# Optimization experiments

Hardware: AMD Instinct MI355X
Metric: run time of the kernel (lower is better)

The kernel has to match this reference:

```python
import math
import jax, jax.numpy as jnp
import numpy as np

B, T, C, H = 4, 1024, 1024, 16


def setup_inputs() -> dict:
    key = jax.random.key(0)
    k1, k2, k3 = jax.random.split(key, 3)
    scale = 0.02
    return {
        "x": jax.random.normal(k1, (B, T, C), dtype=jnp.float32),
        "w_attn": jax.random.normal(k2, (C, 3 * C), dtype=jnp.float32) * scale,
        "b_attn": jnp.zeros((3 * C,), dtype=jnp.float32),
        "w_proj": jax.random.normal(k3, (C, C), dtype=jnp.float32) * scale,
        "b_proj": jnp.zeros((C,), dtype=jnp.float32),
    }


def reference(x, w_attn, b_attn, w_proj, b_proj):
    b, t, c = x.shape
    h = H
    d = c // h
    qkv = x @ w_attn + b_attn                      # [b, t, 3c]
    q, k, v = jnp.split(qkv, 3, axis=-1)
    # [b, h, t, d]
    q = q.reshape(b, t, h, d).transpose(0, 2, 1, 3)
    k = k.reshape(b, t, h, d).transpose(0, 2, 1, 3)
    v = v.reshape(b, t, h, d).transpose(0, 2, 1, 3)
    att = jnp.einsum("bhqd,bhkd->bhqk", q, k) * (1.0 / math.sqrt(d))
    causal = jnp.tril(jnp.ones((t, t), dtype=bool))
    att = jnp.where(causal[None, None], att, -jnp.inf)
    att = jax.nn.softmax(att, axis=-1)
    # dropout is identity in eval mode
    y = jnp.einsum("bhqk,bhkd->bhqd", att, v)      # [b, h, t, d]
    y = y.transpose(0, 2, 1, 3).reshape(b, t, c)
    return y @ w_proj + b_proj
```

## Files before the change

### kernel.cpp

```cpp
#include <hip/hip_runtime.h>

typedef __bf16 bf16;
typedef float f32x4 __attribute__((ext_vector_type(4)));
typedef bf16 bf16x4 __attribute__((ext_vector_type(4)));
typedef bf16 bf16x8 __attribute__((ext_vector_type(8)));

#define MFMA16(a, b, c) __builtin_amdgcn_mfma_f32_16x16x32_bf16((a), (b), (c), 0, 0, 0)

__device__ __forceinline__ f32x4 zero4() {
    f32x4 z; z[0] = 0.f; z[1] = 0.f; z[2] = 0.f; z[3] = 0.f; return z;
}
__device__ __forceinline__ void gl_lds16(const bf16* g, bf16* l) {
    __builtin_amdgcn_global_load_lds(
        (const __attribute__((address_space(1))) void*)g,
        (__attribute__((address_space(3))) void*)l, 16, 0, 0);
}

__global__ __launch_bounds__(256) void conv_k(const float* __restrict__ src,
                                              bf16* __restrict__ dst, int n)
{
    const int i = (blockIdx.x * 256 + threadIdx.x) * 8;
    if (i >= n) return;
    const float4 a = *(const float4*)(src + i);
    const float4 b = *(const float4*)(src + i + 4);
    bf16x8 o;
    o[0] = (bf16)a.x; o[1] = (bf16)a.y; o[2] = (bf16)a.z; o[3] = (bf16)a.w;
    o[4] = (bf16)b.x; o[5] = (bf16)b.y; o[6] = (bf16)b.z; o[7] = (bf16)b.w;
    *(bf16x8*)(dst + i) = o;
}

__global__ __launch_bounds__(256) void transp_k(const float* __restrict__ src,
                                                bf16* __restrict__ dst, int K, int N)
{
    __shared__ bf16 Ls[64][72];
    const int tid = threadIdx.x;
    const int k0 = blockIdx.y << 6;
    const int n0 = blockIdx.x << 6;
    #pragma unroll
    for (int it = 0; it < 4; ++it) {
        const int lin = (it << 10) + (tid << 2);
        const int r = lin >> 6, c = lin & 63;
        const float4 v = *(const float4*)(src + (size_t)(k0 + r) * N + n0 + c);
        bf16x4 o; o[0] = (bf16)v.x; o[1] = (bf16)v.y; o[2] = (bf16)v.z; o[3] = (bf16)v.w;
        *(bf16x4*)&Ls[r][c] = o;
    }
    __syncthreads();
    #pragma unroll
    for (int it = 0; it < 2; ++it) {
        const int lin = (it << 11) + (tid << 3);
        const int nn = lin >> 6, kk = lin & 63;
        bf16x8 o;
        #pragma unroll
        for (int j = 0; j < 8; ++j) o[j] = Ls[kk + j][nn];
        *(bf16x8*)(dst + (size_t)(n0 + nn) * K + k0 + kk) = o;
    }
}

template <int MODE, int BN>
__global__ __launch_bounds__(256)
void gemm_bt(const bf16* __restrict__ A, const bf16* __restrict__ Bt,
             const float* __restrict__ bias,
             bf16* __restrict__ qw, bf16* __restrict__ kw, bf16* __restrict__ vw,
             float* __restrict__ outf, int M, int N, int K)
{
    constexpr int BK = 32;
    constexpr int MF = (BN == 128) ? 4 : 2;
    constexpr int NF = 4;
    constexpr int AE = 128 * BK;
    constexpr int BE = BN * BK;
    constexpr int LPI = (BN == 128) ? 4 : 3;

    __shared__ __align__(16) bf16 smem[3 * (AE + BE)];
    bf16* const Asb = smem;
    bf16* const Bsb = smem + 3 * AE;

    const int tid  = threadIdx.x;
    const int lane = tid & 63;
    const int wid  = tid >> 6;
    const int l16  = lane & 15;
    const int g    = lane >> 4;
    const int wrb  = (BN == 128) ? ((wid >> 1) << 6) : (wid << 5);
    const int wcb  = (BN == 128) ? ((wid & 1) << 6) : 0;

    const int p   = blockIdx.x;
    const int xcd = p & 7;
    const int r   = p >> 3;
    int by, bx;
    if (MODE == 0) { by = ((xcd >> 1) << 3) + r / 12; bx = (xcd & 1) * 12 + r % 12; }
    else           { by = ((xcd >> 1) << 3) + (r >> 3); bx = ((xcd & 1) << 3) + (r & 7); }
    const int m0 = by << 7;
    const int n0 = bx * BN;

    const int srow = lane >> 2;
    const int schk = lane & 3;
    const int rA0 = (wid << 5) + srow;
    const int rA1 = rA0 + 16;
    const int rB0 = wid * (BN / 4) + srow;
    const int rB1 = rB0 + 16;
    const bf16* pa0 = A  + (size_t)(m0 + rA0) * K + ((schk ^ ((rA0 >> 1) & 3)) << 3);
    const bf16* pa1 = A  + (size_t)(m0 + rA1) * K + ((schk ^ ((rA1 >> 1) & 3)) << 3);
    const bf16* pb0 = Bt + (size_t)(n0 + rB0) * K + ((schk ^ ((rB0 >> 1) & 3)) << 3);
    const bf16* pb1 = Bt + (size_t)(n0 + rB1) * K + ((schk ^ ((rB1 >> 1) & 3)) << 3);
    const int dA0 = (wid << 5) * BK, dA1 = dA0 + 16 * BK;
    const int dB0 = (wid * (BN / 4)) * BK, dB1 = dB0 + 16 * BK;

    auto issue = [&](bf16* ab, bf16* bb) {
        gl_lds16(pa0, ab + dA0); gl_lds16(pa1, ab + dA1);
        gl_lds16(pb0, bb + dB0);
        if constexpr (BN == 128) gl_lds16(pb1, bb + dB1);
        pa0 += BK; pa1 += BK; pb0 += BK; pb1 += BK;
    };

    int offA[MF], offB[NF];
    #pragma unroll
    for (int mf = 0; mf < MF; ++mf) {
        const int rr = wrb + (mf << 4) + l16;
        offA[mf] = rr * BK + ((g ^ ((rr >> 1) & 3)) << 3);
    }
    #pragma unroll
    for (int nf = 0; nf < NF; ++nf) {
        const int rr = wcb + (nf << 4) + l16;
        offB[nf] = rr * BK + ((g ^ ((rr >> 1) & 3)) << 3);
    }

    f32x4 acc[MF][NF];
    #pragma unroll
    for (int i = 0; i < MF; ++i)
        #pragma unroll
        for (int j = 0; j < NF; ++j) acc[i][j] = zero4();

    const int nk = K >> 5;
    issue(Asb, Bsb);
    issue(Asb + AE, Bsb + BE);

    for (int kt = 0; kt < nk; ++kt) {
        if (kt == nk - 1) {
            asm volatile("s_waitcnt vmcnt(0)" ::: "memory");
        } else {
            if constexpr (LPI == 4) asm volatile("s_waitcnt vmcnt(4)" ::: "memory");
            else                    asm volatile("s_waitcnt vmcnt(3)" ::: "memory");
        }
        __builtin_amdgcn_s_barrier();
        const int nxt = kt + 2;
        if (nxt < nk) {
            const int s = nxt - (nxt / 3) * 3;
            issue(Asb + s * AE, Bsb + s * BE);
        }
        const int c = kt - (kt / 3) * 3;
        const bf16* ac = Asb + c * AE;
        const bf16* bc = Bsb + c * BE;
        bf16x8 af[MF], bfr[NF];
        #pragma unroll
        for (int mf = 0; mf < MF; ++mf) af[mf] = *(const bf16x8*)&ac[offA[mf]];
        #pragma unroll
        for (int nf = 0; nf < NF; ++nf) bfr[nf] = *(const bf16x8*)&bc[offB[nf]];
        __builtin_amdgcn_s_setprio(1);
        #pragma unroll
        for (int mf = 0; mf < MF; ++mf)
            #pragma unroll
            for (int nf = 0; nf < NF; ++nf)
                acc[mf][nf] = MFMA16(af[mf], bfr[nf], acc[mf][nf]);
        __builtin_amdgcn_s_setprio(0);
    }
    __syncthreads();

    if (MODE == 0) {
        bf16* const Es = smem;
        const int bq  = m0 >> 10;
        const int tb  = m0 & 1023;
        const int hh0 = (n0 & 1023) >> 6;
        const bool isV = (n0 >= 2048);
        if (isV) {
            #pragma unroll
            for (int mf = 0; mf < MF; ++mf)
                #pragma unroll
                for (int nf = 0; nf < NF; ++nf) {
                    const int nn = wcb + (nf << 4) + l16;
                    const float bs = bias[n0 + nn];
                    bf16x4 pq;
                    #pragma unroll
                    for (int j = 0; j < 4; ++j) pq[j] = (bf16)(acc[mf][nf][j] + bs);
                    const int m = wrb + (mf << 4) + (g << 2);
                    const int pp = ((m >> 5) << 5) + (((m >> 2) & 3) << 3) + (((m >> 4) & 1) << 2);
                    *(bf16x4*)&Es[nn * 128 + pp] = pq;
                }
        } else {
            #pragma unroll
            for (int mf = 0; mf < MF; ++mf)
                #pragma unroll
                for (int nf = 0; nf < NF; ++nf) {
                    const int nn = wcb + (nf << 4) + l16;
                    const float bs = bias[n0 + nn];
                    #pragma unroll
                    for (int j = 0; j < 4; ++j) {
                        const int mm = wrb + (mf << 4) + (g << 2) + j;
                        Es[mm * 128 + nn] = (bf16)(acc[mf][nf][j] + bs);
                    }
                }
        }
        __syncthreads();
        #pragma unroll
        for (int it = 0; it < 8; ++it) {
            const int idx = (it << 8) + tid;
            const int row = idx >> 4, ch = idx & 15;
            const bf16x8 v = *(const bf16x8*)&Es[row * 128 + (ch << 3)];
            if (isV) {
                const int dd = row & 63, hh = hh0 + (row >> 6);
                *(bf16x8*)(vw + ((size_t)((bq << 4) + hh) << 16) + ((size_t)dd << 10)
                           + tb + (ch << 3)) = v;
            } else {
                const int t = tb + row;
                const int cc = ch << 3;
                const int hh = hh0 + (cc >> 6);
                bf16* const dst = (n0 < 1024) ? qw : kw;
                *(bf16x8*)(dst + ((size_t)((bq << 4) + hh) << 16) + ((size_t)t << 6)
                           + (cc & 63)) = v;
            }
        }
    } else {
        #pragma unroll
        for (int mf = 0; mf < MF; ++mf)
            #pragma unroll
            for (int nf = 0; nf < NF; ++nf) {
                const int ng = n0 + wcb + (nf << 4) + l16;
                const float bs = bias[ng];
                #pragma unroll
                for (int j = 0; j < 4; ++j) {
                    const int mg = m0 + wrb + (mf << 4) + (g << 2) + j;
                    outf[(size_t)mg * N + ng] = acc[mf][nf][j] + bs;
                }
            }
    }
}

__global__ __launch_bounds__(256)
void attn_k(const bf16* __restrict__ Qp, const bf16* __restrict__ Kp,
            const bf16* __restrict__ Vt, bf16* __restrict__ att)
{
    __shared__ __align__(16) bf16 Kl0[64 * 64], Kl1[64 * 64];
    __shared__ __align__(16) bf16 Vl0[64 * 64], Vl1[64 * 64];

    const int bh = blockIdx.x;
    const int bx = blockIdx.y;
    const int b  = bh >> 4, h = bh & 15;

    const int tid  = threadIdx.x;
    const int lane = tid & 63;
    const int wid  = tid >> 6;
    const int g    = lane >> 4;
    const int l16  = lane & 15;
    const int g8   = g << 3;

    const size_t hb = (size_t)bh << 16;
    const bf16* Qh = Qp + hb;
    const bf16* Kh = Kp + hb;
    const bf16* Vh = Vt + hb;

    const int srow = lane >> 3;
    const int sswz = ((lane & 7) ^ srow) << 3;
    const int kr0  = (wid << 4) + srow;
    const int kr1  = kr0 + 8;
    const int dst0 = (wid << 4) << 6;
    const int dst1 = ((wid << 4) + 8) << 6;

    int offKV[2][4];
    #pragma unroll
    for (int ks = 0; ks < 2; ++ks)
        #pragma unroll
        for (int cb = 0; cb < 4; ++cb) {
            const int r = (cb << 4) + l16;
            offKV[ks][cb] = (r << 6) + (((((ks << 2) + g)) ^ (r & 7)) << 3);
        }

    const float QSCALE = 0.125f * 1.44269504f;

    const int q1b = bx;
    const int q2b = 15 - bx;
    const int nkt = q2b;
    const int qloc = (wid << 4) + l16;

    const bf16* qp1 = Qh + ((size_t)((q1b << 6) + qloc) << 6) + g8;
    const bf16* qp2 = Qh + ((size_t)((q2b << 6) + qloc) << 6) + g8;
    bf16x8 q1f0 = *(const bf16x8*)qp1, q1f1 = *(const bf16x8*)(qp1 + 32);
    bf16x8 q2f0 = *(const bf16x8*)qp2, q2f1 = *(const bf16x8*)(qp2 + 32);
    #pragma unroll
    for (int e = 0; e < 8; ++e) {
        q1f0[e] = (bf16)(QSCALE * (float)q1f0[e]);
        q1f1[e] = (bf16)(QSCALE * (float)q1f1[e]);
        q2f0[e] = (bf16)(QSCALE * (float)q2f0[e]);
        q2f1[e] = (bf16)(QSCALE * (float)q2f1[e]);
    }

    f32x4 acc1[4], acc2[4];
    float m1 = -1e30f, l1 = 0.f, m2 = -1e30f, l2 = 0.f;
    #pragma unroll
    for (int i = 0; i < 4; ++i) { acc1[i] = zero4(); acc2[i] = zero4(); }

    gl_lds16(Kh + ((size_t)kr0 << 6) + sswz, Kl0 + dst0);
    gl_lds16(Kh + ((size_t)kr1 << 6) + sswz, Kl0 + dst1);
    gl_lds16(Vh + ((size_t)kr0 << 10) + sswz, Vl0 + dst0);
    gl_lds16(Vh + ((size_t)kr1 << 10) + sswz, Vl0 + dst1);
    __syncthreads();

    for (int kt = 0; kt <= nkt; ++kt) {
        const bool odd = kt & 1;
        if (kt < nkt) {
            const int kv1 = (kt + 1) << 6;
            bf16* Kn = odd ? Kl0 : Kl1;
            bf16* Vn = odd ? Vl0 : Vl1;
            gl_lds16(Kh + ((size_t)(kv1 + kr0) << 6) + sswz, Kn + dst0);
            gl_lds16(Kh + ((size_t)(kv1 + kr1) << 6) + sswz, Kn + dst1);
            gl_lds16(Vh + ((size_t)kr0 << 10) + kv1 + sswz, Vn + dst0);
            gl_lds16(Vh + ((size_t)kr1 << 10) + kv1 + sswz, Vn + dst1);
        }
        const bf16* Kc = odd ? Kl1 : Kl0;
        const bf16* Vc = odd ? Vl1 : Vl0;

        bf16x8 kf[2][4];
        #pragma unroll
        for (int ks = 0; ks < 2; ++ks)
            #pragma unroll
            for (int cb = 0; cb < 4; ++cb)
                kf[ks][cb] = *(const bf16x8*)&Kc[offKV[ks][cb]];

        {
            f32x4 sacc[4];
            #pragma unroll
            for (int cb = 0; cb < 4; ++cb) sacc[cb] = zero4();
            #pragma unroll
            for (int cb = 0; cb < 4; ++cb) sacc[cb] = MFMA16(kf[0][cb], q2f0, sacc[cb]);
            #pragma unroll
            for (int cb = 0; cb < 4; ++cb) sacc[cb] = MFMA16(kf[1][cb], q2f1, sacc[cb]);
            if (kt == q2b) {
                #pragma unroll
                for (int cb = 0; cb < 4; ++cb)
                    #pragma unroll
                    for (int j = 0; j < 4; ++j)
                        if (((cb << 4) + (g << 2) + j) > qloc) sacc[cb][j] = -1e30f;
            }
            float pm = sacc[0][0];
            #pragma unroll
            for (int cb = 0; cb < 4; ++cb)
                #pragma unroll
                for (int j = 0; j < 4; ++j) pm = fmaxf(pm, sacc[cb][j]);
            pm = fmaxf(pm, __shfl_xor(pm, 16));
            pm = fmaxf(pm, __shfl_xor(pm, 32));
            if (__any(pm > m2 + 8.f)) {
                const float mn = fmaxf(m2, pm);
                const float sc = __builtin_amdgcn_exp2f(m2 - mn);
                m2 = mn; l2 *= sc;
                #pragma unroll
                for (int db = 0; db < 4; ++db)
                    #pragma unroll
                    for (int j = 0; j < 4; ++j) acc2[db][j] *= sc;
            }
            float rsum = 0.f;
            #pragma unroll
            for (int cb = 0; cb < 4; ++cb)
                #pragma unroll
                for (int j = 0; j < 4; ++j) {
                    const float pv = __builtin_amdgcn_exp2f(sacc[cb][j] - m2);
                    sacc[cb][j] = pv;
                    rsum += pv;
                }
            rsum += __shfl_xor(rsum, 16);
            rsum += __shfl_xor(rsum, 32);
            l2 += rsum;
            bf16x8 pf0, pf1;
            #pragma unroll
            for (int i = 0; i < 8; ++i) {
                pf0[i] = (bf16)sacc[i >> 2][i & 3];
                pf1[i] = (bf16)sacc[2 + (i >> 2)][i & 3];
            }
            #pragma unroll
            for (int db = 0; db < 4; ++db) {
                const bf16x8 vf = *(const bf16x8*)&Vc[offKV[0][db]];
                acc2[db] = MFMA16(vf, pf0, acc2[db]);
            }
            #pragma unroll
            for (int db = 0; db < 4; ++db) {
                const bf16x8 vf = *(const bf16x8*)&Vc[offKV[1][db]];
                acc2[db] = MFMA16(vf, pf1, acc2[db]);
            }
        }

        if (kt <= q1b) {
            f32x4 sacc[4];
            #pragma unroll
            for (int cb = 0; cb < 4; ++cb) sacc[cb] = zero4();
            #pragma unroll
            for (int cb = 0; cb < 4; ++cb) sacc[cb] = MFMA16(kf[0][cb], q1f0, sacc[cb]);
            #pragma unroll
            for (int cb = 0; cb < 4; ++cb) sacc[cb] = MFMA16(kf[1][cb], q1f1, sacc[cb]);
            if (kt == q1b) {
                #pragma unroll
                for (int cb = 0; cb < 4; ++cb)
                    #pragma unroll
                    for (int j = 0; j < 4; ++j)
                        if (((cb << 4) + (g << 2) + j) > qloc) sacc[cb][j] = -1e30f;
            }
            float pm = sacc[0][0];
            #pragma unroll
            for (int cb = 0; cb < 4; ++cb)
                #pragma unroll
                for (int j = 0; j < 4; ++j) pm = fmaxf(pm, sacc[cb][j]);
            pm = fmaxf(pm, __shfl_xor(pm, 16));
            pm = fmaxf(pm, __shfl_xor(pm, 32));
            if (__any(pm > m1 + 8.f)) {
                const float mn = fmaxf(m1, pm);
                const float sc = __builtin_amdgcn_exp2f(m1 - mn);
                m1 = mn; l1 *= sc;
                #pragma unroll
                for (int db = 0; db < 4; ++db)
                    #pragma unroll
                    for (int j = 0; j < 4; ++j) acc1[db][j] *= sc;
            }
            float rsum = 0.f;
            #pragma unroll
            for (int cb = 0; cb < 4; ++cb)
                #pragma unroll
                for (int j = 0; j < 4; ++j) {
                    const float pv = __builtin_amdgcn_exp2f(sacc[cb][j] - m1);
                    sacc[cb][j] = pv;
                    rsum += pv;
                }
            rsum += __shfl_xor(rsum, 16);
            rsum += __shfl_xor(rsum, 32);
            l1 += rsum;
            bf16x8 pf0, pf1;
            #pragma unroll
            for (int i = 0; i < 8; ++i) {
                pf0[i] = (bf16)sacc[i >> 2][i & 3];
                pf1[i] = (bf16)sacc[2 + (i >> 2)][i & 3];
            }
            #pragma unroll
            for (int db = 0; db < 4; ++db) {
                const bf16x8 vf = *(const bf16x8*)&Vc[offKV[0][db]];
                acc1[db] = MFMA16(vf, pf0, acc1[db]);
            }
            #pragma unroll
            for (int db = 0; db < 4; ++db) {
                const bf16x8 vf = *(const bf16x8*)&Vc[offKV[1][db]];
                acc1[db] = MFMA16(vf, pf1, acc1[db]);
            }
        }
        __syncthreads();
    }

    {
        const float inv = 1.f / l2;
        const int t = (q2b << 6) + qloc;
        #pragma unroll
        for (int db = 0; db < 4; ++db) {
            bf16x4 o;
            #pragma unroll
            for (int j = 0; j < 4; ++j) o[j] = (bf16)(acc2[db][j] * inv);
            *(bf16x4*)(att + (((size_t)b << 10) + t) * 1024 + (h << 6) + (db << 4) + (g << 2)) = o;
        }
    }
    {
        const float inv = 1.f / l1;
        const int t = (q1b << 6) + qloc;
        #pragma unroll
        for (int db = 0; db < 4; ++db) {
            bf16x4 o;
            #pragma unroll
            for (int j = 0; j < 4; ++j) o[j] = (bf16)(acc1[db][j] * inv);
            *(bf16x4*)(att + (((size_t)b << 10) + t) * 1024 + (h << 6) + (db << 4) + (g << 2)) = o;
        }
    }
}

extern "C" void kernel_launch(void* const* d_in, const int* in_sizes, int n_in,
                              void* d_out, int out_size, void* d_ws, size_t ws_size,
                              hipStream_t stream)
{
    const float* x      = (const float*)d_in[0];
    const float* w_attn = (const float*)d_in[1];
    const float* b_attn = (const float*)d_in[2];
    const float* w_proj = (const float*)d_in[3];
    const float* b_proj = (const float*)d_in[4];
    float* out = (float*)d_out;

    bf16* xb  = (bf16*)d_ws;
    bf16* wT  = xb  + (size_t)4096 * 1024;
    bf16* wpT = wT  + (size_t)3072 * 1024;
    bf16* qw  = wpT + (size_t)1024 * 1024;
    bf16* kw  = qw  + (size_t)64 * 1024 * 64;
    bf16* vw  = kw  + (size_t)64 * 1024 * 64;
    bf16* aw  = vw  + (size_t)64 * 1024 * 64;

    conv_k<<<2048, 256, 0, stream>>>(x, xb, 4096 * 1024);
    transp_k<<<dim3(48, 16), 256, 0, stream>>>(w_attn, wT, 1024, 3072);
    transp_k<<<dim3(16, 16), 256, 0, stream>>>(w_proj, wpT, 1024, 1024);

    gemm_bt<0, 128><<<768, 256, 0, stream>>>(xb, wT, b_attn, qw, kw, vw,
                                             nullptr, 4096, 3072, 1024);
    attn_k<<<dim3(64, 8), 256, 0, stream>>>(qw, kw, vw, aw);
    gemm_bt<1, 64><<<512, 256, 0, stream>>>(aw, wpT, b_proj, nullptr, nullptr, nullptr,
                                            out, 4096, 1024, 1024);
}
```

Before: 91.67 us.

## Merge prep kernels into one launch and use single-buffered BK=64 GEMM loop

Combines the fp32-to-bf16 conversion and both weight transposes into a single prep kernel, removing two launches. The GEMM is changed from a 3-stage async-copy pipeline with BK=32 to a single LDS buffer with BK=64, a wider 8-chunk XOR swizzle, and two syncthreads per K step. This halves the number of K iterations and the LDS footprint, but loses the overlap between global loads and MFMA work, so load latency is exposed on every iteration.

```diff
diff --git a/kernel.cpp b/kernel.cpp
--- a/kernel.cpp
+++ b/kernel.cpp
@@ -16,26 +16,39 @@
         (__attribute__((address_space(3))) void*)l, 16, 0, 0);
 }
 
-__global__ __launch_bounds__(256) void conv_k(const float* __restrict__ src,
-                                              bf16* __restrict__ dst, int n)
-{
-    const int i = (blockIdx.x * 256 + threadIdx.x) * 8;
-    if (i >= n) return;
-    const float4 a = *(const float4*)(src + i);
-    const float4 b = *(const float4*)(src + i + 4);
-    bf16x8 o;
-    o[0] = (bf16)a.x; o[1] = (bf16)a.y; o[2] = (bf16)a.z; o[3] = (bf16)a.w;
-    o[4] = (bf16)b.x; o[5] = (bf16)b.y; o[6] = (bf16)b.z; o[7] = (bf16)b.w;
-    *(bf16x8*)(dst + i) = o;
-}
-
-__global__ __launch_bounds__(256) void transp_k(const float* __restrict__ src,
-                                                bf16* __restrict__ dst, int K, int N)
+__global__ __launch_bounds__(256)
+void prep_k(const float* __restrict__ x, bf16* __restrict__ xb,
+            const float* __restrict__ w_attn, bf16* __restrict__ wT,
+            const float* __restrict__ w_proj, bf16* __restrict__ wpT)
 {
     __shared__ bf16 Ls[64][72];
+    const int blk = blockIdx.x;
     const int tid = threadIdx.x;
-    const int k0 = blockIdx.y << 6;
-    const int n0 = blockIdx.x << 6;
+
+    if (blk < 2048) {
+        const int i = (blk * 256 + tid) * 8;
+        const float4 a = *(const float4*)(x + i);
+        const float4 b = *(const float4*)(x + i + 4);
+        bf16x8 o;
+        o[0] = (bf16)a.x; o[1] = (bf16)a.y; o[2] = (bf16)a.z; o[3] = (bf16)a.w;
+        o[4] = (bf16)b.x; o[5] = (bf16)b.y; o[6] = (bf16)b.z; o[7] = (bf16)b.w;
+        *(bf16x8*)(xb + i) = o;
+        return;
+    }
+    const float* src;
+    bf16* dst;
+    int K, N, bx, by;
+    if (blk < 2816) {
+        const int r = blk - 2048;
+        src = w_attn; dst = wT; K = 1024; N = 3072;
+        bx = r % 48; by = r / 48;
+    } else {
+        const int r = blk - 2816;
+        src = w_proj; dst = wpT; K = 1024; N = 1024;
+        bx = r & 15; by = r >> 4;
+    }
+    const int k0 = by << 6;
+    const int n0 = bx << 6;
     #pragma unroll
     for (int it = 0; it < 4; ++it) {
         const int lin = (it << 10) + (tid << 2);
@@ -56,31 +69,30 @@
     }
 }
 
-template <int MODE, int BN>
+template <int MODE>
 __global__ __launch_bounds__(256)
 void gemm_bt(const bf16* __restrict__ A, const bf16* __restrict__ Bt,
              const float* __restrict__ bias,
              bf16* __restrict__ qw, bf16* __restrict__ kw, bf16* __restrict__ vw,
              float* __restrict__ outf, int M, int N, int K)
 {
-    constexpr int BK = 32;
-    constexpr int MF = (BN == 128) ? 4 : 2;
+    constexpr int BK = 64;
+    constexpr int BN = (MODE == 0) ? 128 : 64;
+    constexpr int MF = (MODE == 0) ? 4 : 2;
     constexpr int NF = 4;
-    constexpr int AE = 128 * BK;
-    constexpr int BE = BN * BK;
-    constexpr int LPI = (BN == 128) ? 4 : 3;
-
-    __shared__ __align__(16) bf16 smem[3 * (AE + BE)];
-    bf16* const Asb = smem;
-    bf16* const Bsb = smem + 3 * AE;
+    constexpr int BI = (MODE == 0) ? 4 : 2;
+
+    __shared__ __align__(16) bf16 smem[128 * BK + BN * BK];
+    bf16* const As = smem;
+    bf16* const Bs = smem + 128 * BK;
 
     const int tid  = threadIdx.x;
     const int lane = tid & 63;
     const int wid  = tid >> 6;
     const int l16  = lane & 15;
     const int g    = lane >> 4;
-    const int wrb  = (BN == 128) ? ((wid >> 1) << 6) : (wid << 5);
-    const int wcb  = (BN == 128) ? ((wid & 1) << 6) : 0;
+    const int wrb  = (MODE == 0) ? ((wid >> 1) << 6) : (wid << 5);
+    const int wcb  = (MODE == 0) ? ((wid & 1) << 6) : 0;
 
     const int p   = blockIdx.x;
     const int xcd = p & 7;
@@ -91,36 +103,37 @@
     const int m0 = by << 7;
     const int n0 = bx * BN;
 
-    const int srow = lane >> 2;
-    const int schk = lane & 3;
-    const int rA0 = (wid << 5) + srow;
-    const int rA1 = rA0 + 16;
-    const int rB0 = wid * (BN / 4) + srow;
-    const int rB1 = rB0 + 16;
-    const bf16* pa0 = A  + (size_t)(m0 + rA0) * K + ((schk ^ ((rA0 >> 1) & 3)) << 3);
-    const bf16* pa1 = A  + (size_t)(m0 + rA1) * K + ((schk ^ ((rA1 >> 1) & 3)) << 3);
-    const bf16* pb0 = Bt + (size_t)(n0 + rB0) * K + ((schk ^ ((rB0 >> 1) & 3)) << 3);
-    const bf16* pb1 = Bt + (size_t)(n0 + rB1) * K + ((schk ^ ((rB1 >> 1) & 3)) << 3);
-    const int dA0 = (wid << 5) * BK, dA1 = dA0 + 16 * BK;
-    const int dB0 = (wid * (BN / 4)) * BK, dB1 = dB0 + 16 * BK;
-
-    auto issue = [&](bf16* ab, bf16* bb) {
-        gl_lds16(pa0, ab + dA0); gl_lds16(pa1, ab + dA1);
-        gl_lds16(pb0, bb + dB0);
-        if constexpr (BN == 128) gl_lds16(pb1, bb + dB1);
-        pa0 += BK; pa1 += BK; pb0 += BK; pb1 += BK;
-    };
-
-    int offA[MF], offB[NF];
-    #pragma unroll
-    for (int mf = 0; mf < MF; ++mf) {
-        const int rr = wrb + (mf << 4) + l16;
-        offA[mf] = rr * BK + ((g ^ ((rr >> 1) & 3)) << 3);
-    }
-    #pragma unroll
-    for (int nf = 0; nf < NF; ++nf) {
-        const int rr = wcb + (nf << 4) + l16;
-        offB[nf] = rr * BK + ((g ^ ((rr >> 1) & 3)) << 3);
+    const int srow = lane >> 3;
+    const int sswz = ((lane & 7) ^ srow) << 3;
+    const bf16* pa[4];
+    const bf16* pb[BI];
+    int dA[4], dB[BI];
+    #pragma unroll
+    for (int i = 0; i < 4; ++i) {
+        const int R = (wid << 5) + (i << 3);
+        pa[i] = A + (size_t)(m0 + R + srow) * K + sswz;
+        dA[i] = R << 6;
+    }
+    #pragma unroll
+    for (int i = 0; i < BI; ++i) {
+        const int R = wid * (BN / 4) + (i << 3);
+        pb[i] = Bt + (size_t)(n0 + R + srow) * K + sswz;
+        dB[i] = R << 6;
+    }
+
+    int offA[2][MF], offB[2][NF];
+    #pragma unroll
+    for (int ks = 0; ks < 2; ++ks) {
+        #pragma unroll
+        for (int mf = 0; mf < MF; ++mf) {
+            const int rr = wrb + (mf << 4) + l16;
+            offA[ks][mf] = (rr << 6) + ((((ks << 2) + g) ^ (rr & 7)) << 3);
+        }
+        #pragma unroll
+        for (int nf = 0; nf < NF; ++nf) {
+            const int rr = wcb + (nf << 4) + l16;
+            offB[ks][nf] = (rr << 6) + ((((ks << 2) + g) ^ (rr & 7)) << 3);
+        }
     }
 
     f32x4 acc[MF][NF];
@@ -129,38 +142,28 @@
         #pragma unroll
         for (int j = 0; j < NF; ++j) acc[i][j] = zero4();
 
-    const int nk = K >> 5;
-    issue(Asb, Bsb);
-    issue(Asb + AE, Bsb + BE);
-
+    const int nk = K >> 6;
     for (int kt = 0; kt < nk; ++kt) {
-        if (kt == nk - 1) {
-            asm volatile("s_waitcnt vmcnt(0)" ::: "memory");
-        } else {
-            if constexpr (LPI == 4) asm volatile("s_waitcnt vmcnt(4)" ::: "memory");
-            else                    asm volatile("s_waitcnt vmcnt(3)" ::: "memory");
-        }
-        __builtin_amdgcn_s_barrier();
-        const int nxt = kt + 2;
-        if (nxt < nk) {
-            const int s = nxt - (nxt / 3) * 3;
-            issue(Asb + s * AE, Bsb + s * BE);
-        }
-        const int c = kt - (kt / 3) * 3;
-        const bf16* ac = Asb + c * AE;
-        const bf16* bc = Bsb + c * BE;
-        bf16x8 af[MF], bfr[NF];
-        #pragma unroll
-        for (int mf = 0; mf < MF; ++mf) af[mf] = *(const bf16x8*)&ac[offA[mf]];
-        #pragma unroll
-        for (int nf = 0; nf < NF; ++nf) bfr[nf] = *(const bf16x8*)&bc[offB[nf]];
-        __builtin_amdgcn_s_setprio(1);
-        #pragma unroll
-        for (int mf = 0; mf < MF; ++mf)
-            #pragma unroll
-            for (int nf = 0; nf < NF; ++nf)
-                acc[mf][nf] = MFMA16(af[mf], bfr[nf], acc[mf][nf]);
-        __builtin_amdgcn_s_setprio(0);
+        const int k0 = kt << 6;
+        __syncthreads();
+        #pragma unroll
+        for (int i = 0; i < 4; ++i)  gl_lds16(pa[i] + k0, As + dA[i]);
+        #pragma unroll
+        for (int i = 0; i < BI; ++i) gl_lds16(pb[i] + k0, Bs + dB[i]);
+        __syncthreads();
+        #pragma unroll
+        for (int ks = 0; ks < 2; ++ks) {
+            bf16x8 af[MF], bfr[NF];
+            #pragma unroll
+            for (int mf = 0; mf < MF; ++mf) af[mf] = *(const bf16x8*)&As[offA[ks][mf]];
+            #pragma unroll
+            for (int nf = 0; nf < NF; ++nf) bfr[nf] = *(const bf16x8*)&Bs[offB[ks][nf]];
+            #pragma unroll
+            for (int mf = 0; mf < MF; ++mf)
+                #pragma unroll
+                for (int nf = 0; nf < NF; ++nf)
+                    acc[mf][nf] = MFMA16(af[mf], bfr[nf], acc[mf][nf]);
+        }
     }
     __syncthreads();
 
@@ -490,13 +493,11 @@
     bf16* vw  = kw  + (size_t)64 * 1024 * 64;
     bf16* aw  = vw  + (size_t)64 * 1024 * 64;
 
-    conv_k<<<2048, 256, 0, stream>>>(x, xb, 4096 * 1024);
-    transp_k<<<dim3(48, 16), 256, 0, stream>>>(w_attn, wT, 1024, 3072);
-    transp_k<<<dim3(16, 16), 256, 0, stream>>>(w_proj, wpT, 1024, 1024);
-
-    gemm_bt<0, 128><<<768, 256, 0, stream>>>(xb, wT, b_attn, qw, kw, vw,
-                                             nullptr, 4096, 3072, 1024);
+    prep_k<<<3072, 256, 0, stream>>>(x, xb, w_attn, wT, w_proj, wpT);
+
+    gemm_bt<0><<<768, 256, 0, stream>>>(xb, wT, b_attn, qw, kw, vw,
+                                        nullptr, 4096, 3072, 1024);
     attn_k<<<dim3(64, 8), 256, 0, stream>>>(qw, kw, vw, aw);
-    gemm_bt<1, 64><<<512, 256, 0, stream>>>(aw, wpT, b_proj, nullptr, nullptr, nullptr,
-                                            out, 4096, 1024, 1024);
+    gemm_bt<1><<<512, 256, 0, stream>>>(aw, wpT, b_proj, nullptr, nullptr, nullptr,
+                                        out, 4096, 1024, 1024);
 }
```

New measurement: 95.99 us. 4.7% more time.
